# Performance work log

Measured on AMD Instinct MI355X. Metric: run time of the kernel, lower is better.

The kernel has to match this reference:

```python
import jax, jax.numpy as jnp
import numpy as np

TEMPERATURE = 0.07
EPS = 1e-8


def setup_inputs() -> dict:
    key = jax.random.key(0)
    k1, k2 = jax.random.split(key)
    B, D = 8192, 256
    embeddings = jax.random.normal(k1, (B, D), dtype=jnp.float32)
    labels = jax.random.randint(k2, (B,), 0, 6, dtype=jnp.int64)
    return {"embeddings": embeddings, "labels": labels}


def reference(embeddings, labels):
    B = embeddings.shape[0]
    # F.normalize(p=2, dim=1): x / max(||x||, eps)
    norm = jnp.linalg.norm(embeddings, axis=1, keepdims=True)
    en = embeddings / jnp.maximum(norm, 1e-12)
    sim = en @ en.T  # [B, B]
    s = sim / TEMPERATURE

    eye = jnp.eye(B, dtype=bool)
    same = labels[:, None] == labels[None, :]
    pos_mask = same & ~eye            # [B, B]
    neg_mask = (~same) & ~eye         # [B, B]

    exp_s = jnp.exp(s)
    # per-row sum of exp over negatives (matches inner-loop denominator term)
    neg_sum = jnp.sum(jnp.where(neg_mask, exp_s, 0.0), axis=1)  # [B]

    # rows contribute only if they have >=1 positive AND >=1 negative
    row_valid = (pos_mask.sum(axis=1) > 0) & (neg_mask.sum(axis=1) > 0)
    pair_mask = pos_mask & row_valid[:, None]

    # -log( exp(s_ij) / (exp(s_ij) + neg_sum_i + 1e-8) ) per positive pair
    per_pair = -jnp.log(exp_s / (exp_s + neg_sum[:, None] + EPS))
    total = jnp.sum(jnp.where(pair_mask, per_pair, 0.0))
    count = jnp.sum(pair_mask)
    loss = jnp.where(count > 0, total / jnp.maximum(count, 1).astype(total.dtype), 0.0)
    return loss
```

## Files before the change

kernel.cpp:

```cpp
#include <hip/hip_runtime.h>
#include <hip/hip_bf16.h>

#define B_ 8192
#define D_ 256
#define TINV 14.285714285714285f
#define EPS_ 1e-8f
#define BK 32
#define NBLK 32
#define NT 64
#define NTRI (NT*(NT+1)/2)

typedef short short8 __attribute__((ext_vector_type(8)));
typedef float f32x4 __attribute__((ext_vector_type(4)));

__device__ __forceinline__ void mfma_bf16(f32x4& acc, short8 a, short8 b) {
    asm("v_mfma_f32_16x16x32_bf16 %0, %1, %2, %0" : "+v"(acc) : "v"(a), "v"(b));
}

__device__ __forceinline__ void mfma_fence() {
    __builtin_amdgcn_sched_barrier(0);
    asm volatile("s_nop 7\ns_nop 7" ::);
}

__device__ __forceinline__ unsigned short f2bf(float x) {
    __hip_bfloat16 h = __float2bfloat16(x);
    return __builtin_bit_cast(unsigned short, h);
}

__device__ __forceinline__ void tri_decode(int idx, int& bi, int& bj) {
    int t = NTRI - 1 - idx;
    int u = (int)((sqrtf(8.f * (float)t + 1.f) - 1.f) * 0.5f);
    while (u * (u + 1) / 2 > t) --u;
    while ((u + 1) * (u + 2) / 2 <= t) ++u;
    bi = (NT - 1) - u;
    bj = (NT - 1) - (t - u * (u + 1) / 2);
}

__device__ __forceinline__ void stage(const char* gbase, int row0, int k0,
                                      short* ldst, int lane, int wid) {
#pragma unroll
    for (int it = 0; it < 2; ++it) {
        int c = (wid << 1) + it;
        int p = (c << 6) + lane;
        int row = p >> 2;
        int kb = (p & 3) ^ ((row >> 1) & 3);
        const char* g = gbase + ((size_t)(row0 + row) * (D_ * 2) + (size_t)(k0 + kb * 8) * 2);
        __builtin_amdgcn_global_load_lds(
            (const __attribute__((address_space(1))) unsigned int*)g,
            (__attribute__((address_space(3))) unsigned int*)(ldst + (size_t)c * 512),
            16, 0, 0);
    }
}

__device__ __forceinline__ void compute_step(const short* lA, const short* lB,
                                             int lane, int wm, int wn, f32x4 acc[4][4]) {
    int rl = lane & 15, kb = lane >> 4;
    short8 a[4], b[4];
#pragma unroll
    for (int m = 0; m < 4; ++m) {
        int row = wm * 64 + m * 16 + rl;
        a[m] = ((const short8*)lA)[row * 4 + (kb ^ ((row >> 1) & 3))];
    }
#pragma unroll
    for (int n = 0; n < 4; ++n) {
        int row = wn * 64 + n * 16 + rl;
        b[n] = ((const short8*)lB)[row * 4 + (kb ^ ((row >> 1) & 3))];
    }
#pragma unroll
    for (int m = 0; m < 4; ++m)
#pragma unroll
        for (int n = 0; n < 4; ++n)
            mfma_bf16(acc[m][n], a[m], b[n]);
}

__device__ __forceinline__ void gemm_pipe(const char* enb, int i0, int j0,
                                          short (*lA)[128 * BK], short (*lB)[128 * BK],
                                          int lane, int wid, int wm, int wn,
                                          f32x4 acc[4][4]) {
    stage(enb, i0, 0, lA[0], lane, wid);
    stage(enb, j0, 0, lB[0], lane, wid);
    stage(enb, i0, BK, lA[1], lane, wid);
    stage(enb, j0, BK, lB[1], lane, wid);
#define PIPE_STEP(T, WAITS)                                                     \
    {                                                                           \
        asm volatile(WAITS ::: "memory");                                       \
        __builtin_amdgcn_sched_barrier(0);                                      \
        __builtin_amdgcn_s_barrier();                                           \
        __builtin_amdgcn_sched_barrier(0);                                      \
        if ((T) + 2 < 8) {                                                      \
            stage(enb, i0, ((T) + 2) * BK, lA[((T) + 2) % 3], lane, wid);       \
            stage(enb, j0, ((T) + 2) * BK, lB[((T) + 2) % 3], lane, wid);       \
        }                                                                       \
        compute_step(lA[(T) % 3], lB[(T) % 3], lane, wm, wn, acc);              \
    }
    PIPE_STEP(0, "s_waitcnt vmcnt(4)")
    PIPE_STEP(1, "s_waitcnt vmcnt(4)")
    PIPE_STEP(2, "s_waitcnt vmcnt(4)")
    PIPE_STEP(3, "s_waitcnt vmcnt(4)")
    PIPE_STEP(4, "s_waitcnt vmcnt(4)")
    PIPE_STEP(5, "s_waitcnt vmcnt(4)")
    PIPE_STEP(6, "s_waitcnt vmcnt(4)")
    PIPE_STEP(7, "s_waitcnt vmcnt(0)")
#undef PIPE_STEP
    mfma_fence();
}

__global__ __launch_bounds__(256) void k_bhist(const int* __restrict__ labels,
                                               unsigned* __restrict__ blockhist,
                                               float* __restrict__ negsum,
                                               float* __restrict__ total) {
    __shared__ unsigned h[8];
    int b = blockIdx.x, t = threadIdx.x;
    if (t < 8) h[t] = 0;
    negsum[b * 256 + t] = 0.f;
    if (b == 0 && t == 0) *total = 0.f;
    __syncthreads();
    atomicAdd(&h[labels[b * 256 + t] & 7], 1u);
    __syncthreads();
    if (t < 8) blockhist[b * 8 + t] = h[t];
}

__global__ __launch_bounds__(256) void k_pos(const int* __restrict__ labels,
                                             const unsigned* __restrict__ blockhist,
                                             unsigned* __restrict__ hist,
                                             int* __restrict__ pos) {
    __shared__ unsigned cnt[8][NBLK];
    __shared__ unsigned clsbase[8];
    __shared__ unsigned wcnt[4][8];
    int b = blockIdx.x, t = threadIdx.x;
    { int bb = t >> 3, c = t & 7; cnt[c][bb] = blockhist[bb * 8 + c]; }
    __syncthreads();
    if (t < 8) {
        unsigned run = 0;
        for (int b2 = 0; b2 < NBLK; ++b2) {
            unsigned v = cnt[t][b2];
            cnt[t][b2] = run;
            run += v;
        }
        clsbase[t] = run;
        if (b == 0) hist[t] = run;
    }
    __syncthreads();
    if (t == 0) {
        unsigned run = 0;
        for (int c = 0; c < 8; ++c) {
            unsigned tot = clsbase[c];
            clsbase[c] = run;
            run += tot;
        }
    }
    __syncthreads();
    int row = b * 256 + t;
    int c = labels[row] & 7;
    int lane = t & 63, w = t >> 6;
    unsigned long long lanebelow = (1ull << lane) - 1ull;
    unsigned myrank = 0;
#pragma unroll
    for (int cv = 0; cv < 8; ++cv) {
        unsigned long long mask = __ballot(c == cv);
        if (lane == 0) wcnt[w][cv] = (unsigned)__popcll(mask);
        if (c == cv) myrank = (unsigned)__popcll(mask & lanebelow);
    }
    __syncthreads();
    unsigned pre = 0;
    for (int wp = 0; wp < 4; ++wp) if (wp < w) pre += wcnt[wp][c];
    pos[row] = (int)(clsbase[c] + cnt[c][b] + pre + myrank);
}

__global__ __launch_bounds__(256) void k_scatter(const float* __restrict__ emb,
                                                 const int* __restrict__ labels,
                                                 const int* __restrict__ pos,
                                                 __hip_bfloat16* __restrict__ en_s,
                                                 int* __restrict__ lab_s) {
    int row = blockIdx.x * 4 + (threadIdx.x >> 6);
    int lane = threadIdx.x & 63;
    float4 v = reinterpret_cast<const float4*>(emb)[(size_t)row * 64 + lane];
    float ss = v.x * v.x + v.y * v.y + v.z * v.z + v.w * v.w;
#pragma unroll
    for (int off = 32; off >= 1; off >>= 1) ss += __shfl_xor(ss, off, 64);
    float scale = 1.0f / fmaxf(sqrtf(ss), 1e-12f);
    int p = pos[row];
    ushort4 o;
    o.x = f2bf(v.x * scale);
    o.y = f2bf(v.y * scale);
    o.z = f2bf(v.z * scale);
    o.w = f2bf(v.w * scale);
    reinterpret_cast<ushort4*>(en_s)[(size_t)p * 64 + lane] = o;
    if (lane == 0) lab_s[p] = labels[row] & 7;
}

template <bool USEP>
__global__ __launch_bounds__(256) void k_negsum(const __hip_bfloat16* __restrict__ en,
                                                const int* __restrict__ lab_s,
                                                float* __restrict__ P,
                                                float* __restrict__ negsum) {
    __shared__ short lA[3][128 * BK];
    __shared__ short lB[3][128 * BK];
    __shared__ int sLi[128], sLj[128];
    int bi, bj;
    tri_decode(blockIdx.x, bi, bj);
    int i0 = bi * 128, j0 = bj * 128;
    int tid = threadIdx.x;
    if (tid < 128) sLi[tid] = lab_s[i0 + tid];
    else           sLj[tid - 128] = lab_s[j0 + tid - 128];
    __syncthreads();

    int lane = tid & 63, wid = tid >> 6;
    int wm = wid >> 1, wn = wid & 1;
    f32x4 acc[4][4] = {};
    gemm_pipe((const char*)en, i0, j0, lA, lB, lane, wid, wm, wn, acc);

    int rl = lane & 15, rowg = (lane >> 4) * 4;
    int lj[4], li[4][4];
#pragma unroll
    for (int n = 0; n < 4; ++n) lj[n] = sLj[wn * 64 + n * 16 + rl];
#pragma unroll
    for (int m = 0; m < 4; ++m)
#pragma unroll
        for (int r = 0; r < 4; ++r) li[m][r] = sLi[wm * 64 + m * 16 + rowg + r];

#pragma unroll
    for (int m = 0; m < 4; ++m)
#pragma unroll
        for (int n = 0; n < 4; ++n)
#pragma unroll
            for (int r = 0; r < 4; ++r)
                acc[m][n][r] = (li[m][r] != lj[n]) ? __expf(acc[m][n][r] * TINV) : 0.f;

    float* sredR = (float*)lA;
    float* sredC = (float*)lB;

#pragma unroll
    for (int m = 0; m < 4; ++m) {
        float part[4];
#pragma unroll
        for (int r = 0; r < 4; ++r)
            part[r] = acc[m][0][r] + acc[m][1][r] + acc[m][2][r] + acc[m][3][r];
#pragma unroll
        for (int off = 1; off < 16; off <<= 1)
#pragma unroll
            for (int r = 0; r < 4; ++r) part[r] += __shfl_xor(part[r], off, 64);
        if (rl == 0) {
#pragma unroll
            for (int r = 0; r < 4; ++r) {
                int row = wm * 64 + m * 16 + rowg + r;
                if (USEP) sredR[wn * 128 + row] = part[r];
                else      atomicAdd(&negsum[i0 + row], part[r]);
            }
        }
    }
    if (bi != bj) {
#pragma unroll
        for (int n = 0; n < 4; ++n) {
            float cp = 0.f;
#pragma unroll
            for (int m = 0; m < 4; ++m)
#pragma unroll
                for (int r = 0; r < 4; ++r) cp += acc[m][n][r];
            cp += __shfl_xor(cp, 16, 64);
            cp += __shfl_xor(cp, 32, 64);
            if (lane < 16) {
                int col = wn * 64 + n * 16 + rl;
                if (USEP) sredC[wm * 128 + col] = cp;
                else      atomicAdd(&negsum[j0 + col], cp);
            }
        }
    }
    if (USEP) {
        __syncthreads();
        if (tid < 128)
            P[(size_t)bj * B_ + i0 + tid] = sredR[tid] + sredR[128 + tid];
        else if (bi != bj)
            P[(size_t)bi * B_ + j0 + (tid - 128)] = sredC[tid - 128] + sredC[128 + (tid - 128)];
    }
}

__global__ __launch_bounds__(256) void k_red(const float* __restrict__ P,
                                             float* __restrict__ negsum) {
    int i = blockIdx.x * 256 + threadIdx.x;
    float s = 0.f;
#pragma unroll 8
    for (int k = 0; k < 64; ++k) s += P[(size_t)k * B_ + i];
    negsum[i] = s;
}

__global__ __launch_bounds__(256) void k_pairs(const __hip_bfloat16* __restrict__ en,
                                               const int* __restrict__ lab_s,
                                               const float* __restrict__ negsum,
                                               const unsigned* __restrict__ hist,
                                               float* __restrict__ total) {
    int bi, bj;
    tri_decode(blockIdx.x, bi, bj);
    int i0 = bi * 128, j0 = bj * 128;
    if (lab_s[j0] > lab_s[i0 + 127]) return;

    __shared__ short lA[3][128 * BK];
    __shared__ short lB[3][128 * BK];
    __shared__ int sLi[128], sLj[128];
    __shared__ float sNgI[128], sNgJ[128];
    int tid = threadIdx.x;
    if (tid < 128) {
        int l = lab_s[i0 + tid];
        unsigned h = hist[l];
        sLi[tid] = (h > 1u && h < (unsigned)B_) ? l : -1;
        sNgI[tid] = negsum[i0 + tid] + EPS_;
    } else {
        int idx = tid - 128;
        int l = lab_s[j0 + idx];
        unsigned h = hist[l];
        sLj[idx] = (h > 1u && h < (unsigned)B_) ? l : -1;
        sNgJ[idx] = negsum[j0 + idx] + EPS_;
    }
    __syncthreads();

    int lane = tid & 63, wid = tid >> 6;
    int wm = wid >> 1, wn = wid & 1;
    f32x4 acc[4][4] = {};
    gemm_pipe((const char*)en, i0, j0, lA, lB, lane, wid, wm, wn, acc);

    int rl = lane & 15, rowg = (lane >> 4) * 4;
    int lj[4];
    float ngJ[4];
#pragma unroll
    for (int n = 0; n < 4; ++n) {
        lj[n] = sLj[wn * 64 + n * 16 + rl];
        ngJ[n] = sNgJ[wn * 64 + n * 16 + rl];
    }

    bool offd = (bi != bj);
    float tot = 0.f;
#pragma unroll
    for (int m = 0; m < 4; ++m) {
#pragma unroll
        for (int r = 0; r < 4; ++r) {
            int ii = wm * 64 + m * 16 + rowg + r;
            int li = sLi[ii];
            float ngI = sNgI[ii];
#pragma unroll
            for (int n = 0; n < 4; ++n) {
                int jj = wn * 64 + n * 16 + rl;
                bool use = (li == lj[n]) && (li >= 0) && (offd || ii != jj);
                if (use) {
                    float s = acc[m][n][r] * TINV;
                    float e = __expf(s);
                    float t = __logf(e + ngI) - s;
                    if (offd) t += __logf(e + ngJ[n]) - s;
                    tot += t;
                }
            }
        }
    }
#pragma unroll
    for (int off = 32; off >= 1; off >>= 1) tot += __shfl_xor(tot, off, 64);
    __shared__ float sred[4];
    if (lane == 0) sred[wid] = tot;
    __syncthreads();
    if (tid == 0) atomicAdd(total, sred[0] + sred[1] + sred[2] + sred[3]);
}

__global__ __launch_bounds__(64) void k_final(const unsigned* __restrict__ hist,
                                              const float* __restrict__ total,
                                              float* __restrict__ out) {
    int t = threadIdx.x;
    unsigned c = 0;
    if (t < 8) {
        unsigned h = hist[t];
        if (h > 1u && h < (unsigned)B_) c = h * (h - 1u);
    }
#pragma unroll
    for (int off = 4; off >= 1; off >>= 1) c += (unsigned)__shfl_xor((int)c, off, 64);
    if (t == 0) out[0] = (c > 0u) ? total[0] / (float)c : 0.f;
}

extern "C" void kernel_launch(void* const* d_in, const int* in_sizes, int n_in,
                              void* d_out, int out_size, void* d_ws, size_t ws_size,
                              hipStream_t stream) {
    const float* emb = (const float*)d_in[0];
    const int* labels = (const int*)d_in[1];
    float* out = (float*)d_out;
    char* ws = (char*)d_ws;

    const size_t EN_BYTES = (size_t)B_ * D_ * 2;
    __hip_bfloat16* en_s = (__hip_bfloat16*)ws;
    char* p = ws + EN_BYTES;
    float* negsum = (float*)p;            p += (size_t)B_ * 4;
    int* lab_s = (int*)p;                 p += (size_t)B_ * 4;
    int* pos = (int*)p;                   p += (size_t)B_ * 4;
    unsigned* blockhist = (unsigned*)p;   p += NBLK * 8 * 4;
    unsigned* hist = (unsigned*)p;        p += 64;
    float* total = (float*)p;             p += 64;
    float* P = (float*)p;
    size_t need = (size_t)(p - ws) + (size_t)NT * B_ * 4;
    bool bigws = ws_size >= need;

    k_bhist<<<NBLK, 256, 0, stream>>>(labels, blockhist, negsum, total);
    k_pos<<<NBLK, 256, 0, stream>>>(labels, blockhist, hist, pos);
    k_scatter<<<B_ / 4, 256, 0, stream>>>(emb, labels, pos, en_s, lab_s);
    if (bigws) {
        k_negsum<true><<<NTRI, 256, 0, stream>>>(en_s, lab_s, P, negsum);
        k_red<<<B_ / 256, 256, 0, stream>>>(P, negsum);
    } else {
        k_negsum<false><<<NTRI, 256, 0, stream>>>(en_s, lab_s, P, negsum);
    }
    k_pairs<<<NTRI, 256, 0, stream>>>(en_s, lab_s, negsum, hist, total);
    k_final<<<1, 64, 0, stream>>>(hist, total, out);
}
```

Before: 77.15 us.

## Keep row tile resident in LDS and sweep four column tiles per block

The negative-sum kernel now loads the full 128x256 A tile into shared memory once and loops over up to four column tiles per block (544 blocks instead of 2080). Row sums stay in registers across tiles and are written with one atomic per row at the end, while column sums use atomics per tile. This drops the partial-sum buffer P and the separate k_red reduction kernel. The cost is fewer blocks, lower occupancy from the larger shared-memory footprint, a simpler double-buffered B pipeline that waits on vmcnt(0) every step, and more atomics on negsum.

```diff
diff --git a/kernel.cpp b/kernel.cpp
--- a/kernel.cpp
+++ b/kernel.cpp
@@ -9,6 +9,7 @@
 #define NBLK 32
 #define NT 64
 #define NTRI (NT*(NT+1)/2)
+#define NGB 544
 
 typedef short short8 __attribute__((ext_vector_type(8)));
 typedef float f32x4 __attribute__((ext_vector_type(4)));
@@ -71,6 +72,106 @@
 #pragma unroll
         for (int n = 0; n < 4; ++n)
             mfma_bf16(acc[m][n], a[m], b[n]);
+}
+
+__global__ __launch_bounds__(256) void k_negsum(const __hip_bfloat16* __restrict__ en,
+                                                const int* __restrict__ lab_s,
+                                                float* __restrict__ negsum) {
+    __shared__ short sA[8][128 * BK];
+    __shared__ short sB[2][128 * BK];
+
+    int b = blockIdx.x;
+    int bi = 0, rem = b;
+    for (; bi < NT; ++bi) {
+        int nc = (NT + 3 - bi) >> 2;
+        if (rem < nc) break;
+        rem -= nc;
+    }
+    int j0t = bi + rem * 4;
+    int njt = min(4, NT - j0t);
+    int i0 = bi * 128;
+
+    int tid = threadIdx.x, lane = tid & 63, wid = tid >> 6;
+    int wm = wid >> 1, wn = wid & 1;
+    int rl = lane & 15, kb = lane >> 4, rowg = kb * 4;
+    const char* enb = (const char*)en;
+
+#pragma unroll
+    for (int t = 0; t < 8; ++t) stage(enb, i0, t * BK, sA[t], lane, wid);
+    stage(enb, j0t * 128, 0, sB[0], lane, wid);
+    unsigned liP[4];
+#pragma unroll
+    for (int m = 0; m < 4; ++m) {
+        unsigned v = 0;
+#pragma unroll
+        for (int r = 0; r < 4; ++r)
+            v |= ((unsigned)lab_s[i0 + wm * 64 + m * 16 + rowg + r] & 7u) << (8 * r);
+        liP[m] = v;
+    }
+    float rsum[4][4] = {};
+    __syncthreads();
+
+    for (int j = 0; j < njt; ++j) {
+        int jj0 = (j0t + j) * 128;
+        f32x4 acc[4][4] = {};
+#pragma unroll
+        for (int t = 0; t < 8; ++t) {
+            asm volatile("s_waitcnt vmcnt(0)" ::: "memory");
+            __builtin_amdgcn_sched_barrier(0);
+            __builtin_amdgcn_s_barrier();
+            __builtin_amdgcn_sched_barrier(0);
+            if (t < 7)
+                stage(enb, jj0, (t + 1) * BK, sB[(t + 1) & 1], lane, wid);
+            else if (j + 1 < njt)
+                stage(enb, jj0 + 128, 0, sB[0], lane, wid);
+            compute_step(sA[t], sB[t & 1], lane, wm, wn, acc);
+        }
+        mfma_fence();
+
+        int lj[4];
+#pragma unroll
+        for (int n = 0; n < 4; ++n) lj[n] = lab_s[jj0 + wn * 64 + n * 16 + rl];
+        float cp[4] = {0.f, 0.f, 0.f, 0.f};
+#pragma unroll
+        for (int m = 0; m < 4; ++m)
+#pragma unroll
+            for (int r = 0; r < 4; ++r) {
+                int li = (int)((liP[m] >> (8 * r)) & 255u);
+#pragma unroll
+                for (int n = 0; n < 4; ++n) {
+                    float e = (li != lj[n]) ? __expf(acc[m][n][r] * TINV) : 0.f;
+                    rsum[m][r] += e;
+                    cp[n] += e;
+                }
+            }
+        if (jj0 != i0) {
+#pragma unroll
+            for (int n = 0; n < 4; ++n) {
+                cp[n] += __shfl_xor(cp[n], 16, 64);
+                cp[n] += __shfl_xor(cp[n], 32, 64);
+            }
+            if (lane < 16) {
+#pragma unroll
+                for (int n = 0; n < 4; ++n)
+                    atomicAdd(&negsum[jj0 + wn * 64 + n * 16 + lane], cp[n]);
+            }
+        }
+    }
+
+#pragma unroll
+    for (int off = 1; off < 16; off <<= 1)
+#pragma unroll
+        for (int m = 0; m < 4; ++m)
+#pragma unroll
+            for (int r = 0; r < 4; ++r)
+                rsum[m][r] += __shfl_xor(rsum[m][r], off, 64);
+    if (rl == 0) {
+#pragma unroll
+        for (int m = 0; m < 4; ++m)
+#pragma unroll
+            for (int r = 0; r < 4; ++r)
+                atomicAdd(&negsum[i0 + wm * 64 + m * 16 + rowg + r], rsum[m][r]);
+    }
 }
 
 __device__ __forceinline__ void gemm_pipe(const char* enb, int i0, int j0,
@@ -189,101 +290,6 @@
     if (lane == 0) lab_s[p] = labels[row] & 7;
 }
 
-template <bool USEP>
-__global__ __launch_bounds__(256) void k_negsum(const __hip_bfloat16* __restrict__ en,
-                                                const int* __restrict__ lab_s,
-                                                float* __restrict__ P,
-                                                float* __restrict__ negsum) {
-    __shared__ short lA[3][128 * BK];
-    __shared__ short lB[3][128 * BK];
-    __shared__ int sLi[128], sLj[128];
-    int bi, bj;
-    tri_decode(blockIdx.x, bi, bj);
-    int i0 = bi * 128, j0 = bj * 128;
-    int tid = threadIdx.x;
-    if (tid < 128) sLi[tid] = lab_s[i0 + tid];
-    else           sLj[tid - 128] = lab_s[j0 + tid - 128];
-    __syncthreads();
-
-    int lane = tid & 63, wid = tid >> 6;
-    int wm = wid >> 1, wn = wid & 1;
-    f32x4 acc[4][4] = {};
-    gemm_pipe((const char*)en, i0, j0, lA, lB, lane, wid, wm, wn, acc);
-
-    int rl = lane & 15, rowg = (lane >> 4) * 4;
-    int lj[4], li[4][4];
-#pragma unroll
-    for (int n = 0; n < 4; ++n) lj[n] = sLj[wn * 64 + n * 16 + rl];
-#pragma unroll
-    for (int m = 0; m < 4; ++m)
-#pragma unroll
-        for (int r = 0; r < 4; ++r) li[m][r] = sLi[wm * 64 + m * 16 + rowg + r];
-
-#pragma unroll
-    for (int m = 0; m < 4; ++m)
-#pragma unroll
-        for (int n = 0; n < 4; ++n)
-#pragma unroll
-            for (int r = 0; r < 4; ++r)
-                acc[m][n][r] = (li[m][r] != lj[n]) ? __expf(acc[m][n][r] * TINV) : 0.f;
-
-    float* sredR = (float*)lA;
-    float* sredC = (float*)lB;
-
-#pragma unroll
-    for (int m = 0; m < 4; ++m) {
-        float part[4];
-#pragma unroll
-        for (int r = 0; r < 4; ++r)
-            part[r] = acc[m][0][r] + acc[m][1][r] + acc[m][2][r] + acc[m][3][r];
-#pragma unroll
-        for (int off = 1; off < 16; off <<= 1)
-#pragma unroll
-            for (int r = 0; r < 4; ++r) part[r] += __shfl_xor(part[r], off, 64);
-        if (rl == 0) {
-#pragma unroll
-            for (int r = 0; r < 4; ++r) {
-                int row = wm * 64 + m * 16 + rowg + r;
-                if (USEP) sredR[wn * 128 + row] = part[r];
-                else      atomicAdd(&negsum[i0 + row], part[r]);
-            }
-        }
-    }
-    if (bi != bj) {
-#pragma unroll
-        for (int n = 0; n < 4; ++n) {
-            float cp = 0.f;
-#pragma unroll
-            for (int m = 0; m < 4; ++m)
-#pragma unroll
-                for (int r = 0; r < 4; ++r) cp += acc[m][n][r];
-            cp += __shfl_xor(cp, 16, 64);
-            cp += __shfl_xor(cp, 32, 64);
-            if (lane < 16) {
-                int col = wn * 64 + n * 16 + rl;
-                if (USEP) sredC[wm * 128 + col] = cp;
-                else      atomicAdd(&negsum[j0 + col], cp);
-            }
-        }
-    }
-    if (USEP) {
-        __syncthreads();
-        if (tid < 128)
-            P[(size_t)bj * B_ + i0 + tid] = sredR[tid] + sredR[128 + tid];
-        else if (bi != bj)
-            P[(size_t)bi * B_ + j0 + (tid - 128)] = sredC[tid - 128] + sredC[128 + (tid - 128)];
-    }
-}
-
-__global__ __launch_bounds__(256) void k_red(const float* __restrict__ P,
-                                             float* __restrict__ negsum) {
-    int i = blockIdx.x * 256 + threadIdx.x;
-    float s = 0.f;
-#pragma unroll 8
-    for (int k = 0; k < 64; ++k) s += P[(size_t)k * B_ + i];
-    negsum[i] = s;
-}
-
 __global__ __launch_bounds__(256) void k_pairs(const __hip_bfloat16* __restrict__ en,
                                                const int* __restrict__ lab_s,
                                                const float* __restrict__ negsum,
@@ -389,19 +395,11 @@
     unsigned* blockhist = (unsigned*)p;   p += NBLK * 8 * 4;
     unsigned* hist = (unsigned*)p;        p += 64;
     float* total = (float*)p;             p += 64;
-    float* P = (float*)p;
-    size_t need = (size_t)(p - ws) + (size_t)NT * B_ * 4;
-    bool bigws = ws_size >= need;
 
     k_bhist<<<NBLK, 256, 0, stream>>>(labels, blockhist, negsum, total);
     k_pos<<<NBLK, 256, 0, stream>>>(labels, blockhist, hist, pos);
     k_scatter<<<B_ / 4, 256, 0, stream>>>(emb, labels, pos, en_s, lab_s);
-    if (bigws) {
-        k_negsum<true><<<NTRI, 256, 0, stream>>>(en_s, lab_s, P, negsum);
-        k_red<<<B_ / 256, 256, 0, stream>>>(P, negsum);
-    } else {
-        k_negsum<false><<<NTRI, 256, 0, stream>>>(en_s, lab_s, P, negsum);
-    }
+    k_negsum<<<NGB, 256, 0, stream>>>(en_s, lab_s, negsum);
     k_pairs<<<NTRI, 256, 0, stream>>>(en_s, lab_s, negsum, hist, total);
     k_final<<<1, 64, 0, stream>>>(hist, total, out);
 }
```

After: 80.44 us. 1.04x slower.

## Cache similarity tiles from negsum pass and reuse them in pair-loss pass

Applied to the files above, without the earlier changes.

The negsum kernel now writes its raw fp32 similarity accumulator tiles for label-overlapping tile pairs to a workspace buffer. A new pair kernel reads those tiles instead of recomputing the bf16 GEMM, so the second matrix multiply is skipped. The exp/mask and row/column reductions are also fused into one loop. The cost is extra global writes and reads of 64KB per stored tile, and a larger workspace requirement that falls back to the old path if it is not met.

```diff
diff --git a/kernel.cpp b/kernel.cpp
--- a/kernel.cpp
+++ b/kernel.cpp
@@ -189,11 +189,12 @@
     if (lane == 0) lab_s[p] = labels[row] & 7;
 }
 
-template <bool USEP>
+template <bool USEP, bool STORES>
 __global__ __launch_bounds__(256) void k_negsum(const __hip_bfloat16* __restrict__ en,
                                                 const int* __restrict__ lab_s,
                                                 float* __restrict__ P,
-                                                float* __restrict__ negsum) {
+                                                float* __restrict__ negsum,
+                                                float* __restrict__ S) {
     __shared__ short lA[3][128 * BK];
     __shared__ short lB[3][128 * BK];
     __shared__ int sLi[128], sLj[128];
@@ -210,6 +211,15 @@
     f32x4 acc[4][4] = {};
     gemm_pipe((const char*)en, i0, j0, lA, lB, lane, wid, wm, wn, acc);
 
+    if (STORES && sLj[0] <= sLi[127]) {
+        f32x4* Ss = (f32x4*)(S + (size_t)blockIdx.x * 16384);
+#pragma unroll
+        for (int m = 0; m < 4; ++m)
+#pragma unroll
+            for (int n = 0; n < 4; ++n)
+                Ss[(m * 4 + n) * 256 + tid] = acc[m][n];
+    }
+
     int rl = lane & 15, rowg = (lane >> 4) * 4;
     int lj[4], li[4][4];
 #pragma unroll
@@ -219,23 +229,23 @@
 #pragma unroll
         for (int r = 0; r < 4; ++r) li[m][r] = sLi[wm * 64 + m * 16 + rowg + r];
 
-#pragma unroll
-    for (int m = 0; m < 4; ++m)
-#pragma unroll
-        for (int n = 0; n < 4; ++n)
-#pragma unroll
-            for (int r = 0; r < 4; ++r)
-                acc[m][n][r] = (li[m][r] != lj[n]) ? __expf(acc[m][n][r] * TINV) : 0.f;
-
     float* sredR = (float*)lA;
     float* sredC = (float*)lB;
 
+    float cp[4] = {0.f, 0.f, 0.f, 0.f};
 #pragma unroll
     for (int m = 0; m < 4; ++m) {
         float part[4];
 #pragma unroll
-        for (int r = 0; r < 4; ++r)
-            part[r] = acc[m][0][r] + acc[m][1][r] + acc[m][2][r] + acc[m][3][r];
+        for (int r = 0; r < 4; ++r) {
+            part[r] = 0.f;
+#pragma unroll
+            for (int n = 0; n < 4; ++n) {
+                float e = (li[m][r] != lj[n]) ? __expf(acc[m][n][r] * TINV) : 0.f;
+                part[r] += e;
+                cp[n] += e;
+            }
+        }
 #pragma unroll
         for (int off = 1; off < 16; off <<= 1)
 #pragma unroll
@@ -252,17 +262,12 @@
     if (bi != bj) {
 #pragma unroll
         for (int n = 0; n < 4; ++n) {
-            float cp = 0.f;
-#pragma unroll
-            for (int m = 0; m < 4; ++m)
-#pragma unroll
-                for (int r = 0; r < 4; ++r) cp += acc[m][n][r];
-            cp += __shfl_xor(cp, 16, 64);
-            cp += __shfl_xor(cp, 32, 64);
+            cp[n] += __shfl_xor(cp[n], 16, 64);
+            cp[n] += __shfl_xor(cp[n], 32, 64);
             if (lane < 16) {
                 int col = wn * 64 + n * 16 + rl;
-                if (USEP) sredC[wm * 128 + col] = cp;
-                else      atomicAdd(&negsum[j0 + col], cp);
+                if (USEP) sredC[wm * 128 + col] = cp[n];
+                else      atomicAdd(&negsum[j0 + col], cp[n]);
             }
         }
     }
@@ -282,6 +287,77 @@
 #pragma unroll 8
     for (int k = 0; k < 64; ++k) s += P[(size_t)k * B_ + i];
     negsum[i] = s;
+}
+
+__global__ __launch_bounds__(256) void k_pairs2(const float* __restrict__ S,
+                                                const int* __restrict__ lab_s,
+                                                const float* __restrict__ negsum,
+                                                const unsigned* __restrict__ hist,
+                                                float* __restrict__ total) {
+    int bi, bj;
+    tri_decode(blockIdx.x, bi, bj);
+    int i0 = bi * 128, j0 = bj * 128;
+    if (lab_s[j0] > lab_s[i0 + 127]) return;
+
+    __shared__ int sLi[128], sLj[128];
+    __shared__ float sNgI[128], sNgJ[128];
+    int tid = threadIdx.x;
+    if (tid < 128) {
+        int l = lab_s[i0 + tid];
+        unsigned h = hist[l];
+        sLi[tid] = (h > 1u && h < (unsigned)B_) ? l : -1;
+        sNgI[tid] = negsum[i0 + tid] + EPS_;
+    } else {
+        int idx = tid - 128;
+        int l = lab_s[j0 + idx];
+        unsigned h = hist[l];
+        sLj[idx] = (h > 1u && h < (unsigned)B_) ? l : -1;
+        sNgJ[idx] = negsum[j0 + idx] + EPS_;
+    }
+    __syncthreads();
+
+    int lane = tid & 63, wid = tid >> 6;
+    int wm = wid >> 1, wn = wid & 1;
+    int rl = lane & 15, rowg = (lane >> 4) * 4;
+    const f32x4* Ss = (const f32x4*)(S + (size_t)blockIdx.x * 16384);
+
+    int lj[4];
+    float ngJ[4];
+#pragma unroll
+    for (int n = 0; n < 4; ++n) {
+        lj[n] = sLj[wn * 64 + n * 16 + rl];
+        ngJ[n] = sNgJ[wn * 64 + n * 16 + rl];
+    }
+
+    bool offd = (bi != bj);
+    float tot = 0.f;
+#pragma unroll
+    for (int m = 0; m < 4; ++m) {
+#pragma unroll
+        for (int n = 0; n < 4; ++n) {
+            f32x4 v = Ss[(m * 4 + n) * 256 + tid];
+#pragma unroll
+            for (int r = 0; r < 4; ++r) {
+                int ii = wm * 64 + m * 16 + rowg + r;
+                int li = sLi[ii];
+                int jj = wn * 64 + n * 16 + rl;
+                bool use = (li == lj[n]) && (li >= 0) && (offd || ii != jj);
+                if (use) {
+                    float s = v[r] * TINV;
+                    float e = __expf(s);
+                    float t = __logf(e + sNgI[ii]) - s;
+                    if (offd) t += __logf(e + ngJ[n]) - s;
+                    tot += t;
+                }
+            }
+        }
+    }
+#pragma unroll
+    for (int off = 32; off >= 1; off >>= 1) tot += __shfl_xor(tot, off, 64);
+    __shared__ float sred[4];
+    if (lane == 0) sred[wid] = tot;
+    __syncthreads();
+    if (tid == 0) atomicAdd(total, sred[0] + sred[1] + sred[2] + sred[3]);
 }
 
 __global__ __launch_bounds__(256) void k_pairs(const __hip_bfloat16* __restrict__ en,
@@ -389,19 +465,21 @@
     unsigned* blockhist = (unsigned*)p;   p += NBLK * 8 * 4;
     unsigned* hist = (unsigned*)p;        p += 64;
     float* total = (float*)p;             p += 64;
-    float* P = (float*)p;
-    size_t need = (size_t)(p - ws) + (size_t)NT * B_ * 4;
+    float* P = (float*)p;                 p += (size_t)NT * B_ * 4;
+    float* S = (float*)p;
+    size_t need = (size_t)(p - ws) + (size_t)NTRI * 16384 * 4;
     bool bigws = ws_size >= need;
 
     k_bhist<<<NBLK, 256, 0, stream>>>(labels, blockhist, negsum, total);
     k_pos<<<NBLK, 256, 0, stream>>>(labels, blockhist, hist, pos);
     k_scatter<<<B_ / 4, 256, 0, stream>>>(emb, labels, pos, en_s, lab_s);
     if (bigws) {
-        k_negsum<true><<<NTRI, 256, 0, stream>>>(en_s, lab_s, P, negsum);
+        k_negsum<true, true><<<NTRI, 256, 0, stream>>>(en_s, lab_s, P, negsum, S);
         k_red<<<B_ / 256, 256, 0, stream>>>(P, negsum);
+        k_pairs2<<<NTRI, 256, 0, stream>>>(S, lab_s, negsum, hist, total);
     } else {
-        k_negsum<false><<<NTRI, 256, 0, stream>>>(en_s, lab_s, P, negsum);
-    }
-    k_pairs<<<NTRI, 256, 0, stream>>>(en_s, lab_s, negsum, hist, total);
+        k_negsum<false, false><<<NTRI, 256, 0, stream>>>(en_s, lab_s, P, negsum, S);
+        k_pairs<<<NTRI, 256, 0, stream>>>(en_s, lab_s, negsum, hist, total);
+    }
     k_final<<<1, 64, 0, stream>>>(hist, total, out);
 }
```

Result: slower. 79.98 us (+3.7%).

## Split 128x128 tiles across eight waves and fuse exp with row/column reductions

Applied to the files above, without the earlier changes.

The negsum and pairs GEMM kernels now launch 512 threads, so eight waves each own a 32x64 sub-tile instead of four waves with 64x64. This halves the accumulator registers per wave and halves the staging loads per thread, which should allow more waves to stay resident and hide latency better. The exp is now computed and summed into row and column partials in one pass instead of overwriting the accumulators first. The cost is more waves sharing each barrier, more shared-memory reduction slots, and a larger per-block reduction in P.

```diff
diff --git a/kernel.cpp b/kernel.cpp
--- a/kernel.cpp
+++ b/kernel.cpp
@@ -38,27 +38,23 @@
 
 __device__ __forceinline__ void stage(const char* gbase, int row0, int k0,
                                       short* ldst, int lane, int wid) {
-#pragma unroll
-    for (int it = 0; it < 2; ++it) {
-        int c = (wid << 1) + it;
-        int p = (c << 6) + lane;
-        int row = p >> 2;
-        int kb = (p & 3) ^ ((row >> 1) & 3);
-        const char* g = gbase + ((size_t)(row0 + row) * (D_ * 2) + (size_t)(k0 + kb * 8) * 2);
-        __builtin_amdgcn_global_load_lds(
-            (const __attribute__((address_space(1))) unsigned int*)g,
-            (__attribute__((address_space(3))) unsigned int*)(ldst + (size_t)c * 512),
-            16, 0, 0);
-    }
+    int p = (wid << 6) + lane;
+    int row = p >> 2;
+    int kb = (p & 3) ^ ((row >> 1) & 3);
+    const char* g = gbase + ((size_t)(row0 + row) * (D_ * 2) + (size_t)(k0 + kb * 8) * 2);
+    __builtin_amdgcn_global_load_lds(
+        (const __attribute__((address_space(1))) unsigned int*)g,
+        (__attribute__((address_space(3))) unsigned int*)(ldst + ((size_t)wid << 9)),
+        16, 0, 0);
 }
 
 __device__ __forceinline__ void compute_step(const short* lA, const short* lB,
-                                             int lane, int wm, int wn, f32x4 acc[4][4]) {
+                                             int lane, int wm, int wn, f32x4 acc[2][4]) {
     int rl = lane & 15, kb = lane >> 4;
-    short8 a[4], b[4];
-#pragma unroll
-    for (int m = 0; m < 4; ++m) {
-        int row = wm * 64 + m * 16 + rl;
+    short8 a[2], b[4];
+#pragma unroll
+    for (int m = 0; m < 2; ++m) {
+        int row = wm * 32 + m * 16 + rl;
         a[m] = ((const short8*)lA)[row * 4 + (kb ^ ((row >> 1) & 3))];
     }
 #pragma unroll
@@ -67,7 +63,7 @@
         b[n] = ((const short8*)lB)[row * 4 + (kb ^ ((row >> 1) & 3))];
     }
 #pragma unroll
-    for (int m = 0; m < 4; ++m)
+    for (int m = 0; m < 2; ++m)
 #pragma unroll
         for (int n = 0; n < 4; ++n)
             mfma_bf16(acc[m][n], a[m], b[n]);
@@ -76,7 +72,7 @@
 __device__ __forceinline__ void gemm_pipe(const char* enb, int i0, int j0,
                                           short (*lA)[128 * BK], short (*lB)[128 * BK],
                                           int lane, int wid, int wm, int wn,
-                                          f32x4 acc[4][4]) {
+                                          f32x4 acc[2][4]) {
     stage(enb, i0, 0, lA[0], lane, wid);
     stage(enb, j0, 0, lB[0], lane, wid);
     stage(enb, i0, BK, lA[1], lane, wid);
@@ -93,13 +89,13 @@
         }                                                                       \
         compute_step(lA[(T) % 3], lB[(T) % 3], lane, wm, wn, acc);              \
     }
-    PIPE_STEP(0, "s_waitcnt vmcnt(4)")
-    PIPE_STEP(1, "s_waitcnt vmcnt(4)")
-    PIPE_STEP(2, "s_waitcnt vmcnt(4)")
-    PIPE_STEP(3, "s_waitcnt vmcnt(4)")
-    PIPE_STEP(4, "s_waitcnt vmcnt(4)")
-    PIPE_STEP(5, "s_waitcnt vmcnt(4)")
-    PIPE_STEP(6, "s_waitcnt vmcnt(4)")
+    PIPE_STEP(0, "s_waitcnt vmcnt(2)")
+    PIPE_STEP(1, "s_waitcnt vmcnt(2)")
+    PIPE_STEP(2, "s_waitcnt vmcnt(2)")
+    PIPE_STEP(3, "s_waitcnt vmcnt(2)")
+    PIPE_STEP(4, "s_waitcnt vmcnt(2)")
+    PIPE_STEP(5, "s_waitcnt vmcnt(2)")
+    PIPE_STEP(6, "s_waitcnt vmcnt(2)")
     PIPE_STEP(7, "s_waitcnt vmcnt(0)")
 #undef PIPE_STEP
     mfma_fence();
@@ -190,10 +186,10 @@
 }
 
 template <bool USEP>
-__global__ __launch_bounds__(256) void k_negsum(const __hip_bfloat16* __restrict__ en,
-                                                const int* __restrict__ lab_s,
-                                                float* __restrict__ P,
-                                                float* __restrict__ negsum) {
+__global__ __launch_bounds__(512, 6) void k_negsum(const __hip_bfloat16* __restrict__ en,
+                                                   const int* __restrict__ lab_s,
+                                                   float* __restrict__ P,
+                                                   float* __restrict__ negsum) {
     __shared__ short lA[3][128 * BK];
     __shared__ short lB[3][128 * BK];
     __shared__ int sLi[128], sLj[128];
@@ -202,40 +198,40 @@
     int i0 = bi * 128, j0 = bj * 128;
     int tid = threadIdx.x;
     if (tid < 128) sLi[tid] = lab_s[i0 + tid];
-    else           sLj[tid - 128] = lab_s[j0 + tid - 128];
+    else if (tid < 256) sLj[tid - 128] = lab_s[j0 + tid - 128];
     __syncthreads();
 
     int lane = tid & 63, wid = tid >> 6;
     int wm = wid >> 1, wn = wid & 1;
-    f32x4 acc[4][4] = {};
+    f32x4 acc[2][4] = {};
     gemm_pipe((const char*)en, i0, j0, lA, lB, lane, wid, wm, wn, acc);
 
     int rl = lane & 15, rowg = (lane >> 4) * 4;
-    int lj[4], li[4][4];
+    int lj[4], li[2][4];
 #pragma unroll
     for (int n = 0; n < 4; ++n) lj[n] = sLj[wn * 64 + n * 16 + rl];
 #pragma unroll
-    for (int m = 0; m < 4; ++m)
-#pragma unroll
-        for (int r = 0; r < 4; ++r) li[m][r] = sLi[wm * 64 + m * 16 + rowg + r];
-
-#pragma unroll
-    for (int m = 0; m < 4; ++m)
-#pragma unroll
-        for (int n = 0; n < 4; ++n)
-#pragma unroll
-            for (int r = 0; r < 4; ++r)
-                acc[m][n][r] = (li[m][r] != lj[n]) ? __expf(acc[m][n][r] * TINV) : 0.f;
+    for (int m = 0; m < 2; ++m)
+#pragma unroll
+        for (int r = 0; r < 4; ++r) li[m][r] = sLi[wm * 32 + m * 16 + rowg + r];
 
     float* sredR = (float*)lA;
     float* sredC = (float*)lB;
 
-#pragma unroll
-    for (int m = 0; m < 4; ++m) {
+    float cp[4] = {0.f, 0.f, 0.f, 0.f};
+#pragma unroll
+    for (int m = 0; m < 2; ++m) {
         float part[4];
 #pragma unroll
-        for (int r = 0; r < 4; ++r)
-            part[r] = acc[m][0][r] + acc[m][1][r] + acc[m][2][r] + acc[m][3][r];
+        for (int r = 0; r < 4; ++r) {
+            part[r] = 0.f;
+#pragma unroll
+            for (int n = 0; n < 4; ++n) {
+                float e = (li[m][r] != lj[n]) ? __expf(acc[m][n][r] * TINV) : 0.f;
+                part[r] += e;
+                cp[n] += e;
+            }
+        }
 #pragma unroll
         for (int off = 1; off < 16; off <<= 1)
 #pragma unroll
@@ -243,7 +239,7 @@
         if (rl == 0) {
 #pragma unroll
             for (int r = 0; r < 4; ++r) {
-                int row = wm * 64 + m * 16 + rowg + r;
+                int row = wm * 32 + m * 16 + rowg + r;
                 if (USEP) sredR[wn * 128 + row] = part[r];
                 else      atomicAdd(&negsum[i0 + row], part[r]);
             }
@@ -252,17 +248,12 @@
     if (bi != bj) {
 #pragma unroll
         for (int n = 0; n < 4; ++n) {
-            float cp = 0.f;
-#pragma unroll
-            for (int m = 0; m < 4; ++m)
-#pragma unroll
-                for (int r = 0; r < 4; ++r) cp += acc[m][n][r];
-            cp += __shfl_xor(cp, 16, 64);
-            cp += __shfl_xor(cp, 32, 64);
+            cp[n] += __shfl_xor(cp[n], 16, 64);
+            cp[n] += __shfl_xor(cp[n], 32, 64);
             if (lane < 16) {
-                int col = wn * 64 + n * 16 + rl;
-                if (USEP) sredC[wm * 128 + col] = cp;
-                else      atomicAdd(&negsum[j0 + col], cp);
+                int col = wn * 64 + n * 16 + lane;
+                if (USEP) sredC[wm * 128 + col] = cp[n];
+                else      atomicAdd(&negsum[j0 + col], cp[n]);
             }
         }
     }
@@ -270,8 +261,11 @@
         __syncthreads();
         if (tid < 128)
             P[(size_t)bj * B_ + i0 + tid] = sredR[tid] + sredR[128 + tid];
-        else if (bi != bj)
-            P[(size_t)bi * B_ + j0 + (tid - 128)] = sredC[tid - 128] + sredC[128 + (tid - 128)];
+        else if (tid < 256 && bi != bj) {
+            int c = tid - 128;
+            P[(size_t)bi * B_ + j0 + c] =
+                sredC[c] + sredC[128 + c] + sredC[256 + c] + sredC[384 + c];
+        }
     }
 }
 
@@ -284,11 +278,11 @@
     negsum[i] = s;
 }
 
-__global__ __launch_bounds__(256) void k_pairs(const __hip_bfloat16* __restrict__ en,
-                                               const int* __restrict__ lab_s,
-                                               const float* __restrict__ negsum,
-                                               const unsigned* __restrict__ hist,
-                                               float* __restrict__ total) {
+__global__ __launch_bounds__(512, 6) void k_pairs(const __hip_bfloat16* __restrict__ en,
+                                                  const int* __restrict__ lab_s,
+                                                  const float* __restrict__ negsum,
+                                                  const unsigned* __restrict__ hist,
+                                                  float* __restrict__ total) {
     int bi, bj;
     tri_decode(blockIdx.x, bi, bj);
     int i0 = bi * 128, j0 = bj * 128;
@@ -304,7 +298,7 @@
         unsigned h = hist[l];
         sLi[tid] = (h > 1u && h < (unsigned)B_) ? l : -1;
         sNgI[tid] = negsum[i0 + tid] + EPS_;
-    } else {
+    } else if (tid < 256) {
         int idx = tid - 128;
         int l = lab_s[j0 + idx];
         unsigned h = hist[l];
@@ -315,7 +309,7 @@
 
     int lane = tid & 63, wid = tid >> 6;
     int wm = wid >> 1, wn = wid & 1;
-    f32x4 acc[4][4] = {};
+    f32x4 acc[2][4] = {};
     gemm_pipe((const char*)en, i0, j0, lA, lB, lane, wid, wm, wn, acc);
 
     int rl = lane & 15, rowg = (lane >> 4) * 4;
@@ -330,10 +324,10 @@
     bool offd = (bi != bj);
     float tot = 0.f;
 #pragma unroll
-    for (int m = 0; m < 4; ++m) {
+    for (int m = 0; m < 2; ++m) {
 #pragma unroll
         for (int r = 0; r < 4; ++r) {
-            int ii = wm * 64 + m * 16 + rowg + r;
+            int ii = wm * 32 + m * 16 + rowg + r;
             int li = sLi[ii];
             float ngI = sNgI[ii];
 #pragma unroll
@@ -352,10 +346,15 @@
     }
 #pragma unroll
     for (int off = 32; off >= 1; off >>= 1) tot += __shfl_xor(tot, off, 64);
-    __shared__ float sred[4];
+    __shared__ float sred[8];
     if (lane == 0) sred[wid] = tot;
     __syncthreads();
-    if (tid == 0) atomicAdd(total, sred[0] + sred[1] + sred[2] + sred[3]);
+    if (tid == 0) {
+        float s = 0.f;
+#pragma unroll
+        for (int w = 0; w < 8; ++w) s += sred[w];
+        atomicAdd(total, s);
+    }
 }
 
 __global__ __launch_bounds__(64) void k_final(const unsigned* __restrict__ hist,
@@ -397,11 +396,11 @@
     k_pos<<<NBLK, 256, 0, stream>>>(labels, blockhist, hist, pos);
     k_scatter<<<B_ / 4, 256, 0, stream>>>(emb, labels, pos, en_s, lab_s);
     if (bigws) {
-        k_negsum<true><<<NTRI, 256, 0, stream>>>(en_s, lab_s, P, negsum);
+        k_negsum<true><<<NTRI, 512, 0, stream>>>(en_s, lab_s, P, negsum);
         k_red<<<B_ / 256, 256, 0, stream>>>(P, negsum);
     } else {
-        k_negsum<false><<<NTRI, 256, 0, stream>>>(en_s, lab_s, P, negsum);
-    }
-    k_pairs<<<NTRI, 256, 0, stream>>>(en_s, lab_s, negsum, hist, total);
+        k_negsum<false><<<NTRI, 512, 0, stream>>>(en_s, lab_s, P, negsum);
+    }
+    k_pairs<<<NTRI, 512, 0, stream>>>(en_s, lab_s, negsum, hist, total);
     k_final<<<1, 64, 0, stream>>>(hist, total, out);
 }
```

Result: faster. 74.00 us (-4.1%).
